# Performance work log

Hardware: AMD Instinct MI355X
Metric: run time of the kernel (lower is better)

The kernel has to match this reference:

```python
import jax, jax.numpy as jnp
import numpy as np

B, T, D, H = 2, 2048, 1024, 16
HD = D // H  # head_dim = 64


def setup_inputs() -> dict:
    key = jax.random.key(0)
    ks = jax.random.split(key, 6)
    x = jax.random.normal(ks[0], (B, T, D), dtype=jnp.float32)
    wq = jax.random.normal(ks[1], (D, D), dtype=jnp.float32) * (D ** -0.5)
    wk = jax.random.normal(ks[2], (D, D), dtype=jnp.float32) * (D ** -0.5)
    wv = jax.random.normal(ks[3], (D, D), dtype=jnp.float32) * (D ** -0.5)
    wo = jax.random.normal(ks[4], (D, D), dtype=jnp.float32) * (D ** -0.5)
    # RoPE tables: standard inverse-frequency angles, shape [T, head_dim]
    inv_freq = 1.0 / (10000.0 ** (jnp.arange(0, HD, 2, dtype=jnp.float32) / HD))
    ang = jnp.arange(T, dtype=jnp.float32)[:, None] * inv_freq[None, :]  # [T, HD/2]
    ang = jnp.concatenate([ang, ang], axis=-1)  # [T, HD]
    cos, sin = jnp.cos(ang), jnp.sin(ang)
    # causal mask [1,1,T,T]: True where attention is allowed
    mask = jnp.tril(jnp.ones((T, T), dtype=bool))[None, None]
    return {"x": x, "wq": wq, "wk": wk, "wv": wv, "wo": wo,
            "cos": cos, "sin": sin, "mask": mask}


def rotate_half(u):
    u1, u2 = jnp.split(u, 2, axis=-1)
    return jnp.concatenate([-u2, u1], axis=-1)


def reference(x, wq, wk, wv, wo, cos, sin, mask):
    b, t, c = x.shape
    # projections (nn.Linear: y = x @ W^T), reshape to [B, H, T, HD]
    def proj(w):
        return (x @ w.T).reshape(b, t, H, HD).transpose(0, 2, 1, 3)
    q, k, v = proj(wq), proj(wk), proj(wv)
    # inline RoPE: cos/sin broadcast [1,1,T,HD]
    co = cos[:t][None, None]
    si = sin[:t][None, None]
    q = q * co + rotate_half(q) * si
    k = k * co + rotate_half(k) * si
    # scaled dot-product attention with causal mask
    att = jnp.einsum("bhqd,bhkd->bhqk", q, k) * (HD ** -0.5)
    att = jnp.where(mask[:, :, :t, :t], att, -jnp.inf)
    att = jax.nn.softmax(att, axis=-1)
    out = jnp.einsum("bhqk,bhkd->bhqd", att, v)
    out = out.transpose(0, 2, 1, 3).reshape(b, t, c)
    return out @ wo.T
```

## Files before the change

### kernel.cpp

```cpp
#include <hip/hip_runtime.h>
#include <hip/hip_bf16.h>
#include <type_traits>

#define B_  2
#define T_  2048
#define D_  1024
#define H_  16
#define HD_ 64

typedef __attribute__((ext_vector_type(8))) short bf16x8;
typedef __attribute__((ext_vector_type(4))) float f32x4;

__device__ __forceinline__ unsigned short f2b(float x) {
  union { __hip_bfloat16 h; unsigned short u; } c;
  c.h = __float2bfloat16(x);
  return c.u;
}
__device__ __forceinline__ float b2f(unsigned short u) {
  union { unsigned short u; __hip_bfloat16 h; } c;
  c.u = u;
  return __bfloat162float(c.h);
}

__device__ __forceinline__ void ld_g2l_16(const unsigned short* g, unsigned short* l) {
  auto gp = (const __attribute__((address_space(1))) unsigned int*)g;
  auto lp = (__attribute__((address_space(3))) unsigned int*)l;
  __builtin_amdgcn_global_load_lds(gp, lp, 16, 0, 0);
}

__global__ void __launch_bounds__(256)
cast_all(const float* __restrict__ x, const float* __restrict__ wq,
         const float* __restrict__ wk, const float* __restrict__ wv,
         const float* __restrict__ wo, unsigned short* __restrict__ xb,
         unsigned short* __restrict__ wp) {
  int blk = blockIdx.x;
  const float* src;
  unsigned short* dst;
  size_t off;
  if (blk < 2048) {
    src = x; dst = xb; off = (size_t)blk * 2048;
  } else {
    int t = (blk - 2048) >> 9;
    int r = (blk - 2048) & 511;
    src = (t == 0) ? wq : (t == 1) ? wk : (t == 2) ? wv : wo;
    dst = wp + (size_t)t * 1048576;
    off = (size_t)r * 2048;
  }
  size_t i = off + threadIdx.x * 8;
  float4 a = *(const float4*)(src + i);
  float4 b = *(const float4*)(src + i + 4);
  unsigned short h[8] = {f2b(a.x), f2b(a.y), f2b(a.z), f2b(a.w),
                         f2b(b.x), f2b(b.y), f2b(b.z), f2b(b.w)};
  *(uint4*)(dst + i) = *(uint4*)h;
}

template <typename OutT, int MROWS>
__device__ __forceinline__ void gemm_core(const unsigned short* __restrict__ A,
                                          const unsigned short* __restrict__ Bw,
                                          OutT* __restrict__ C, int K, int Ldc,
                                          int rope_mode, const float* __restrict__ cosT,
                                          const float* __restrict__ sinT, int tok0) {
  constexpr int MT = MROWS / 32;
  __shared__ unsigned short a_s[2][MROWS * 32];
  __shared__ unsigned short b_s[2][128 * 32];
  const int tid = threadIdx.x;
  const int lane = tid & 63;
  const int w = tid >> 6;
  const int m16 = lane & 15;
  const int quad = lane >> 4;
  const int wm = w >> 1, wn = w & 1;
  const int rl = lane >> 2;
  const int cl = (lane & 3) * 8;

  f32x4 acc[MT][4];
#pragma unroll
  for (int i = 0; i < MT; i++)
#pragma unroll
    for (int j = 0; j < 4; j++) acc[i][j] = (f32x4){0.f, 0.f, 0.f, 0.f};

  auto stage = [&](int it, int bs) {
    int k0 = it * 32;
#pragma unroll
    for (int t = 0; t < MROWS / 64; t++) {
      int seg = w * 16 + t * 64;
      ld_g2l_16(A + (size_t)(seg + rl) * K + k0 + cl, &a_s[bs][seg * 32]);
    }
#pragma unroll
    for (int j2 = 0; j2 < 2; j2++) {
      int seg = w * 32 + j2 * 16;
      ld_g2l_16(Bw + (size_t)(seg + rl) * K + k0 + cl, &b_s[bs][seg * 32]);
    }
  };

  const int nit = K / 32;
  stage(0, 0);
  __syncthreads();
  for (int it = 0; it < nit; it++) {
    int cur = it & 1;
    if (it + 1 < nit) stage(it + 1, cur ^ 1);
    bf16x8 af[MT], bfr[4];
#pragma unroll
    for (int mt = 0; mt < MT; mt++)
      af[mt] = *(const bf16x8*)&a_s[cur][(wm * (MT * 16) + mt * 16 + m16) * 32 + quad * 8];
#pragma unroll
    for (int nt = 0; nt < 4; nt++)
      bfr[nt] = *(const bf16x8*)&b_s[cur][(wn * 64 + nt * 16 + m16) * 32 + quad * 8];
#pragma unroll
    for (int mt = 0; mt < MT; mt++)
#pragma unroll
      for (int nt = 0; nt < 4; nt++)
        acc[mt][nt] = __builtin_amdgcn_mfma_f32_16x16x32_bf16(af[mt], bfr[nt], acc[mt][nt], 0, 0, 0);
    __syncthreads();
  }

  if (rope_mode) {
    float scale = (rope_mode == 2) ? 0.18033688011112042f : 1.f;
#pragma unroll
    for (int mt = 0; mt < MT; mt++)
#pragma unroll
      for (int reg = 0; reg < 4; reg++) {
        int t = (tok0 + wm * (MT * 16) + mt * 16 + quad * 4 + reg) & (T_ - 1);
#pragma unroll
        for (int nt = 0; nt < 2; nt++) {
          int d = nt * 16 + m16;
          float co = cosT[t * HD_ + d] * scale;
          float si = sinT[t * HD_ + d] * scale;
          float lo = acc[mt][nt][reg], hi = acc[mt][nt + 2][reg];
          acc[mt][nt][reg]     = lo * co - hi * si;
          acc[mt][nt + 2][reg] = hi * co + lo * si;
        }
      }
  }
#pragma unroll
  for (int mt = 0; mt < MT; mt++)
#pragma unroll
    for (int nt = 0; nt < 4; nt++)
#pragma unroll
      for (int reg = 0; reg < 4; reg++) {
        OutT* p = C + (size_t)(wm * (MT * 16) + mt * 16 + quad * 4 + reg) * Ldc + wn * 64 + nt * 16 + m16;
        if constexpr (std::is_same_v<OutT, float>) *p = acc[mt][nt][reg];
        else *p = f2b(acc[mt][nt][reg]);
      }
}

__global__ void __launch_bounds__(256)
gemm_qkv(const unsigned short* __restrict__ xb, const unsigned short* __restrict__ wp,
         unsigned short* __restrict__ qkv, const float* __restrict__ cosT,
         const float* __restrict__ sinT) {
  const int nb = blockIdx.x;
  const int bm = blockIdx.y * 128;
  const int mi = nb >> 3;
  const int bn = (nb & 7) * 128;
  const int rope_mode = (mi == 0) ? 2 : (mi == 1) ? 1 : 0;
  gemm_core<unsigned short, 128>(xb + (size_t)bm * D_,
                                 wp + (size_t)(mi * 1024 + bn) * D_,
                                 qkv + (size_t)mi * (4096ull * D_) + (size_t)bm * D_ + bn,
                                 D_, D_, rope_mode, cosT, sinT, bm);
}

__global__ void __launch_bounds__(256)
gemm_out(const unsigned short* __restrict__ Ab, const unsigned short* __restrict__ wob,
         float* __restrict__ C) {
  const int bn = blockIdx.x * 128;
  const int bm = blockIdx.y * 64;
  gemm_core<float, 64>(Ab + (size_t)bm * D_, wob + (size_t)bn * D_,
                       C + (size_t)bm * D_ + bn, D_, D_, 0, nullptr, nullptr, 0);
}

__global__ void __launch_bounds__(256)
vtrans(const unsigned short* __restrict__ V, unsigned short* __restrict__ VT) {
  __shared__ unsigned short tile[64][72];
  const int tid = threadIdx.x;
  const int tb = blockIdx.x, h = blockIdx.y, b = blockIdx.z;
  const unsigned short* Vb = V + ((size_t)b * T_ + tb * 64) * D_ + h * HD_;
  int r = tid >> 2;
  int c = (tid & 3) * 16;
  bf16x8 v0 = *(const bf16x8*)(Vb + (size_t)r * D_ + c);
  bf16x8 v1 = *(const bf16x8*)(Vb + (size_t)r * D_ + c + 8);
#pragma unroll
  for (int e = 0; e < 8; e++) tile[c + e][r] = ((unsigned short*)&v0)[e];
#pragma unroll
  for (int e = 0; e < 8; e++) tile[c + 8 + e][r] = ((unsigned short*)&v1)[e];
  __syncthreads();
  unsigned short* VTb = VT + ((size_t)b * H_ + h) * HD_ * T_ + tb * 64;
  *(bf16x8*)(VTb + (size_t)r * T_ + c)     = *(const bf16x8*)&tile[r][c];
  *(bf16x8*)(VTb + (size_t)r * T_ + c + 8) = *(const bf16x8*)&tile[r][c + 8];
}

__global__ void __launch_bounds__(256, 3)
attn_kernel(const unsigned short* __restrict__ Q, const unsigned short* __restrict__ K,
            const unsigned short* __restrict__ VT, unsigned short* __restrict__ O) {
  __shared__ __align__(16) unsigned short qp_s[64][72];
  __shared__ __align__(16) unsigned short k_s[2][64 * 64];
  __shared__ __align__(16) unsigned short vt_s[2][64 * 64];

  const int tid = threadIdx.x;
  const int lane = tid & 63;
  const int w = tid >> 6;
  const int m16 = lane & 15;
  const int quad = lane >> 4;
  const int swz = m16 & 7;
  const int pc0 = quad ^ swz;
  const int pc1 = pc0 ^ 4;

  const int x = blockIdx.x;
  const int qt = 31 - (x >> 5);
  const int bh = x & 31;
  const int b = bh >> 4, h = bh & 15;
  const int q0 = qt * 64;

  const unsigned short* Qb = Q + ((size_t)b * T_ + q0) * D_ + h * HD_;
  const unsigned short* Kb = K + (size_t)b * T_ * D_ + h * HD_;
  const unsigned short* VTb = VT + ((size_t)b * H_ + h) * HD_ * T_;

#pragma unroll
  for (int i = 0; i < 2; i++) {
    int idx = tid + i * 256;
    int r = idx >> 3, c = idx & 7;
    *(bf16x8*)&qp_s[r][c * 8] = *(const bf16x8*)(Qb + (size_t)r * D_ + c * 8);
  }

  auto stage_kv = [&](int kt, int bs) {
    int rs = lane >> 3;
    int cs = ((lane & 7) ^ rs) * 8;
    int gr = w * 16 + rs;
    ld_g2l_16(Kb + (size_t)(kt * 64 + gr) * D_ + cs,      &k_s[bs][(w * 16) * 64]);
    ld_g2l_16(Kb + (size_t)(kt * 64 + gr + 8) * D_ + cs,  &k_s[bs][(w * 16 + 8) * 64]);
    ld_g2l_16(VTb + (size_t)gr * T_ + kt * 64 + cs,       &vt_s[bs][(w * 16) * 64]);
    ld_g2l_16(VTb + (size_t)(gr + 8) * T_ + kt * 64 + cs, &vt_s[bs][(w * 16 + 8) * 64]);
  };

  f32x4 o_acc[4];
#pragma unroll
  for (int dt = 0; dt < 4; dt++) o_acc[dt] = (f32x4){0.f, 0.f, 0.f, 0.f};
  float m_i = -1e30f, l_i = 0.f;
  const int rg = q0 + w * 16 + m16;

  stage_kv(0, 0);
  __syncthreads();
  bf16x8 q_frag[2];
  q_frag[0] = *(const bf16x8*)&qp_s[w * 16 + m16][quad * 8];
  q_frag[1] = *(const bf16x8*)&qp_s[w * 16 + m16][32 + quad * 8];

  for (int t = 0; t <= qt; t++) {
    int cur = t & 1;
    if (t < qt) stage_kv(t + 1, cur ^ 1);

    const unsigned short* kc = &k_s[cur][0];
    const unsigned short* vc = &vt_s[cur][0];
    f32x4 sf[4];
    __builtin_amdgcn_s_setprio(1);
#pragma unroll
    for (int jt = 0; jt < 4; jt++) {
      bf16x8 a0 = *(const bf16x8*)&kc[(jt * 16 + m16) * 64 + pc0 * 8];
      bf16x8 a1 = *(const bf16x8*)&kc[(jt * 16 + m16) * 64 + pc1 * 8];
      f32x4 acc = (f32x4){0.f, 0.f, 0.f, 0.f};
      acc = __builtin_amdgcn_mfma_f32_16x16x32_bf16(a0, q_frag[0], acc, 0, 0, 0);
      acc = __builtin_amdgcn_mfma_f32_16x16x32_bf16(a1, q_frag[1], acc, 0, 0, 0);
      sf[jt] = acc;
    }
    __builtin_amdgcn_s_setprio(0);
    if (t == qt) {
#pragma unroll
      for (int jt = 0; jt < 4; jt++)
#pragma unroll
        for (int reg = 0; reg < 4; reg++) {
          int jg = t * 64 + jt * 16 + quad * 4 + reg;
          if (jg > rg) sf[jt][reg] = -1e30f;
        }
    }
    float mx = sf[0][0];
#pragma unroll
    for (int jt = 0; jt < 4; jt++)
#pragma unroll
      for (int reg = 0; reg < 4; reg++) mx = fmaxf(mx, sf[jt][reg]);
    mx = fmaxf(mx, __shfl_xor(mx, 16, 64));
    mx = fmaxf(mx, __shfl_xor(mx, 32, 64));
    if (!__all(mx <= m_i + 8.f)) {
      float mn = fmaxf(m_i, mx);
      float alpha = exp2f(m_i - mn);
      l_i *= alpha;
#pragma unroll
      for (int dt = 0; dt < 4; dt++)
#pragma unroll
        for (int reg = 0; reg < 4; reg++) o_acc[dt][reg] *= alpha;
      m_i = mn;
    }
    float lt = 0.f;
    float p[4][4];
#pragma unroll
    for (int jt = 0; jt < 4; jt++)
#pragma unroll
      for (int reg = 0; reg < 4; reg++) {
        p[jt][reg] = exp2f(sf[jt][reg] - m_i);
        lt += p[jt][reg];
      }
#pragma unroll
    for (int jt = 0; jt < 4; jt++) {
      unsigned short pk[4] = {f2b(p[jt][0]), f2b(p[jt][1]), f2b(p[jt][2]), f2b(p[jt][3])};
      *(uint2*)&qp_s[w * 16 + m16][jt * 16 + quad * 4] = *(uint2*)pk;
    }
    bf16x8 bp0 = *(const bf16x8*)&qp_s[w * 16 + m16][quad * 8];
    bf16x8 bp1 = *(const bf16x8*)&qp_s[w * 16 + m16][32 + quad * 8];
    __builtin_amdgcn_s_setprio(1);
#pragma unroll
    for (int dt = 0; dt < 4; dt++) {
      int rowd = dt * 16 + m16;
      bf16x8 a0 = *(const bf16x8*)&vc[rowd * 64 + pc0 * 8];
      bf16x8 a1 = *(const bf16x8*)&vc[rowd * 64 + pc1 * 8];
      o_acc[dt] = __builtin_amdgcn_mfma_f32_16x16x32_bf16(a0, bp0, o_acc[dt], 0, 0, 0);
      o_acc[dt] = __builtin_amdgcn_mfma_f32_16x16x32_bf16(a1, bp1, o_acc[dt], 0, 0, 0);
    }
    __builtin_amdgcn_s_setprio(0);
    lt += __shfl_xor(lt, 16, 64);
    lt += __shfl_xor(lt, 32, 64);
    l_i += lt;
    __syncthreads();
  }

  float inv = 1.f / l_i;
#pragma unroll
  for (int dt = 0; dt < 4; dt++) {
    unsigned short ok[4];
#pragma unroll
    for (int reg = 0; reg < 4; reg++) ok[reg] = f2b(o_acc[dt][reg] * inv);
    *(uint2*)&qp_s[w * 16 + m16][dt * 16 + quad * 4] = *(uint2*)ok;
  }
  __syncthreads();
  unsigned short* Ob = O + ((size_t)b * T_ + q0) * D_ + h * HD_;
#pragma unroll
  for (int i = 0; i < 2; i++) {
    int idx = tid + i * 256;
    int r = idx >> 3, c = idx & 7;
    *(bf16x8*)(Ob + (size_t)r * D_ + c * 8) = *(const bf16x8*)&qp_s[r][c * 8];
  }
}

extern "C" void kernel_launch(void* const* d_in, const int* in_sizes, int n_in,
                              void* d_out, int out_size, void* d_ws, size_t ws_size,
                              hipStream_t stream) {
  const float* x    = (const float*)d_in[0];
  const float* wq   = (const float*)d_in[1];
  const float* wk   = (const float*)d_in[2];
  const float* wv   = (const float*)d_in[3];
  const float* wo   = (const float*)d_in[4];
  const float* cosT = (const float*)d_in[5];
  const float* sinT = (const float*)d_in[6];
  float* out = (float*)d_out;

  const size_t NTOK = (size_t)B_ * T_;
  const size_t SZ   = NTOK * D_;
  unsigned short* xb   = (unsigned short*)d_ws;
  unsigned short* Wp   = xb + SZ;
  unsigned short* QKVh = Wp + 4 * 1048576;
  unsigned short* Ab   = QKVh + 3 * SZ;
  unsigned short* VTb  = xb;

  cast_all<<<4096, 256, 0, stream>>>(x, wq, wk, wv, wo, xb, Wp);
  gemm_qkv<<<dim3(24, 32), 256, 0, stream>>>(xb, Wp, QKVh, cosT, sinT);
  vtrans<<<dim3(32, 16, 2), 256, 0, stream>>>(QKVh + 2 * SZ, VTb);
  attn_kernel<<<1024, 256, 0, stream>>>(QKVh, QKVh + SZ, VTb, Ab);
  gemm_out<<<dim3(8, 64), 256, 0, stream>>>(Ab, Wp + 3 * 1048576, out);
}
```

Measured before the change: 203.2 us.

## Enlarge attention query tile to 128 rows with two sub-tiles per wave

Each attention block now handles 128 query rows instead of 64, and each wave owns 32 rows split into two 16-row sub-tiles. This lets every K/V tile staged in shared memory serve twice as many queries and halves the block count. Block-to-tile mapping is changed to pair long and short causal tiles across the two halves of the grid, and waves whose rows sit entirely before the current key tile skip compute. The cost is more registers per wave, which may lower occupancy, plus uneven per-wave work near the diagonal.

```diff
diff --git a/kernel.cpp b/kernel.cpp
--- a/kernel.cpp
+++ b/kernel.cpp
@@ -190,7 +190,7 @@
 __global__ void __launch_bounds__(256, 3)
 attn_kernel(const unsigned short* __restrict__ Q, const unsigned short* __restrict__ K,
             const unsigned short* __restrict__ VT, unsigned short* __restrict__ O) {
-  __shared__ __align__(16) unsigned short qp_s[64][72];
+  __shared__ __align__(16) unsigned short qp_s[128][72];
   __shared__ __align__(16) unsigned short k_s[2][64 * 64];
   __shared__ __align__(16) unsigned short vt_s[2][64 * 64];
 
@@ -204,20 +204,21 @@
   const int pc1 = pc0 ^ 4;
 
   const int x = blockIdx.x;
-  const int qt = 31 - (x >> 5);
-  const int bh = x & 31;
+  const int c = x & 255, half = x >> 8;
+  const int bh = c & 31, jj = c >> 5;
+  const int qt = half ? jj : 15 - jj;
   const int b = bh >> 4, h = bh & 15;
-  const int q0 = qt * 64;
+  const int q0 = qt * 128;
 
   const unsigned short* Qb = Q + ((size_t)b * T_ + q0) * D_ + h * HD_;
   const unsigned short* Kb = K + (size_t)b * T_ * D_ + h * HD_;
   const unsigned short* VTb = VT + ((size_t)b * H_ + h) * HD_ * T_;
 
 #pragma unroll
-  for (int i = 0; i < 2; i++) {
+  for (int i = 0; i < 4; i++) {
     int idx = tid + i * 256;
-    int r = idx >> 3, c = idx & 7;
-    *(bf16x8*)&qp_s[r][c * 8] = *(const bf16x8*)(Qb + (size_t)r * D_ + c * 8);
+    int r = idx >> 3, cc = idx & 7;
+    *(bf16x8*)&qp_s[r][cc * 8] = *(const bf16x8*)(Qb + (size_t)r * D_ + cc * 8);
   }
 
   auto stage_kv = [&](int kt, int bs) {
@@ -230,109 +231,148 @@
     ld_g2l_16(VTb + (size_t)(gr + 8) * T_ + kt * 64 + cs, &vt_s[bs][(w * 16 + 8) * 64]);
   };
 
-  f32x4 o_acc[4];
-#pragma unroll
-  for (int dt = 0; dt < 4; dt++) o_acc[dt] = (f32x4){0.f, 0.f, 0.f, 0.f};
-  float m_i = -1e30f, l_i = 0.f;
-  const int rg = q0 + w * 16 + m16;
+  f32x4 o_acc[2][4];
+#pragma unroll
+  for (int s = 0; s < 2; s++)
+#pragma unroll
+    for (int dt = 0; dt < 4; dt++) o_acc[s][dt] = (f32x4){0.f, 0.f, 0.f, 0.f};
+  float m_i[2] = {-1e30f, -1e30f}, l_i[2] = {0.f, 0.f};
+  const int rg0 = q0 + w * 32 + m16;
+  const int ktmax = 2 * qt + 1;
 
   stage_kv(0, 0);
   __syncthreads();
-  bf16x8 q_frag[2];
-  q_frag[0] = *(const bf16x8*)&qp_s[w * 16 + m16][quad * 8];
-  q_frag[1] = *(const bf16x8*)&qp_s[w * 16 + m16][32 + quad * 8];
-
-  for (int t = 0; t <= qt; t++) {
+  bf16x8 q_frag[2][2];
+#pragma unroll
+  for (int s = 0; s < 2; s++) {
+    q_frag[s][0] = *(const bf16x8*)&qp_s[w * 32 + s * 16 + m16][quad * 8];
+    q_frag[s][1] = *(const bf16x8*)&qp_s[w * 32 + s * 16 + m16][32 + quad * 8];
+  }
+
+  for (int t = 0; t <= ktmax; t++) {
     int cur = t & 1;
-    if (t < qt) stage_kv(t + 1, cur ^ 1);
-
-    const unsigned short* kc = &k_s[cur][0];
-    const unsigned short* vc = &vt_s[cur][0];
-    f32x4 sf[4];
-    __builtin_amdgcn_s_setprio(1);
-#pragma unroll
-    for (int jt = 0; jt < 4; jt++) {
-      bf16x8 a0 = *(const bf16x8*)&kc[(jt * 16 + m16) * 64 + pc0 * 8];
-      bf16x8 a1 = *(const bf16x8*)&kc[(jt * 16 + m16) * 64 + pc1 * 8];
-      f32x4 acc = (f32x4){0.f, 0.f, 0.f, 0.f};
-      acc = __builtin_amdgcn_mfma_f32_16x16x32_bf16(a0, q_frag[0], acc, 0, 0, 0);
-      acc = __builtin_amdgcn_mfma_f32_16x16x32_bf16(a1, q_frag[1], acc, 0, 0, 0);
-      sf[jt] = acc;
+    if (t < ktmax) stage_kv(t + 1, cur ^ 1);
+
+    if (t * 64 <= q0 + w * 32 + 31) {
+      const unsigned short* kc = &k_s[cur][0];
+      const unsigned short* vc = &vt_s[cur][0];
+      f32x4 sf[2][4];
+      __builtin_amdgcn_s_setprio(1);
+#pragma unroll
+      for (int jt = 0; jt < 4; jt++) {
+        bf16x8 a0 = *(const bf16x8*)&kc[(jt * 16 + m16) * 64 + pc0 * 8];
+        bf16x8 a1 = *(const bf16x8*)&kc[(jt * 16 + m16) * 64 + pc1 * 8];
+#pragma unroll
+        for (int s = 0; s < 2; s++) {
+          f32x4 acc = (f32x4){0.f, 0.f, 0.f, 0.f};
+          acc = __builtin_amdgcn_mfma_f32_16x16x32_bf16(a0, q_frag[s][0], acc, 0, 0, 0);
+          acc = __builtin_amdgcn_mfma_f32_16x16x32_bf16(a1, q_frag[s][1], acc, 0, 0, 0);
+          sf[s][jt] = acc;
+        }
+      }
+      __builtin_amdgcn_s_setprio(0);
+      if (t * 64 + 63 > q0 + w * 32) {
+#pragma unroll
+        for (int s = 0; s < 2; s++) {
+          int rg = rg0 + s * 16;
+#pragma unroll
+          for (int jt = 0; jt < 4; jt++)
+#pragma unroll
+            for (int reg = 0; reg < 4; reg++) {
+              int jg = t * 64 + jt * 16 + quad * 4 + reg;
+              if (jg > rg) sf[s][jt][reg] = -1e30f;
+            }
+        }
+      }
+      float mx[2];
+#pragma unroll
+      for (int s = 0; s < 2; s++) {
+        float m = sf[s][0][0];
+#pragma unroll
+        for (int jt = 0; jt < 4; jt++)
+#pragma unroll
+          for (int reg = 0; reg < 4; reg++) m = fmaxf(m, sf[s][jt][reg]);
+        m = fmaxf(m, __shfl_xor(m, 16, 64));
+        m = fmaxf(m, __shfl_xor(m, 32, 64));
+        mx[s] = m;
+      }
+      if (!__all(fmaxf(mx[0] - m_i[0], mx[1] - m_i[1]) <= 8.f)) {
+#pragma unroll
+        for (int s = 0; s < 2; s++) {
+          float mn = fmaxf(m_i[s], mx[s]);
+          float alpha = exp2f(m_i[s] - mn);
+          l_i[s] *= alpha;
+#pragma unroll
+          for (int dt = 0; dt < 4; dt++)
+#pragma unroll
+            for (int reg = 0; reg < 4; reg++) o_acc[s][dt][reg] *= alpha;
+          m_i[s] = mn;
+        }
+      }
+      float lt[2] = {0.f, 0.f};
+#pragma unroll
+      for (int s = 0; s < 2; s++) {
+        float p[4][4];
+#pragma unroll
+        for (int jt = 0; jt < 4; jt++)
+#pragma unroll
+          for (int reg = 0; reg < 4; reg++) {
+            p[jt][reg] = exp2f(sf[s][jt][reg] - m_i[s]);
+            lt[s] += p[jt][reg];
+          }
+#pragma unroll
+        for (int jt = 0; jt < 4; jt++) {
+          unsigned short pk[4] = {f2b(p[jt][0]), f2b(p[jt][1]), f2b(p[jt][2]), f2b(p[jt][3])};
+          *(uint2*)&qp_s[w * 32 + s * 16 + m16][jt * 16 + quad * 4] = *(uint2*)pk;
+        }
+      }
+      bf16x8 bp[2][2];
+#pragma unroll
+      for (int s = 0; s < 2; s++) {
+        bp[s][0] = *(const bf16x8*)&qp_s[w * 32 + s * 16 + m16][quad * 8];
+        bp[s][1] = *(const bf16x8*)&qp_s[w * 32 + s * 16 + m16][32 + quad * 8];
+      }
+      __builtin_amdgcn_s_setprio(1);
+#pragma unroll
+      for (int dt = 0; dt < 4; dt++) {
+        int rowd = dt * 16 + m16;
+        bf16x8 a0 = *(const bf16x8*)&vc[rowd * 64 + pc0 * 8];
+        bf16x8 a1 = *(const bf16x8*)&vc[rowd * 64 + pc1 * 8];
+#pragma unroll
+        for (int s = 0; s < 2; s++) {
+          o_acc[s][dt] = __builtin_amdgcn_mfma_f32_16x16x32_bf16(a0, bp[s][0], o_acc[s][dt], 0, 0, 0);
+          o_acc[s][dt] = __builtin_amdgcn_mfma_f32_16x16x32_bf16(a1, bp[s][1], o_acc[s][dt], 0, 0, 0);
+        }
+      }
+      __builtin_amdgcn_s_setprio(0);
+#pragma unroll
+      for (int s = 0; s < 2; s++) {
+        lt[s] += __shfl_xor(lt[s], 16, 64);
+        lt[s] += __shfl_xor(lt[s], 32, 64);
+        l_i[s] += lt[s];
+      }
     }
-    __builtin_amdgcn_s_setprio(0);
-    if (t == qt) {
-#pragma unroll
-      for (int jt = 0; jt < 4; jt++)
-#pragma unroll
-        for (int reg = 0; reg < 4; reg++) {
-          int jg = t * 64 + jt * 16 + quad * 4 + reg;
-          if (jg > rg) sf[jt][reg] = -1e30f;
-        }
+    __syncthreads();
+  }
+
+#pragma unroll
+  for (int s = 0; s < 2; s++) {
+    float inv = 1.f / l_i[s];
+#pragma unroll
+    for (int dt = 0; dt < 4; dt++) {
+      unsigned short ok[4];
+#pragma unroll
+      for (int reg = 0; reg < 4; reg++) ok[reg] = f2b(o_acc[s][dt][reg] * inv);
+      *(uint2*)&qp_s[w * 32 + s * 16 + m16][dt * 16 + quad * 4] = *(uint2*)ok;
     }
-    float mx = sf[0][0];
-#pragma unroll
-    for (int jt = 0; jt < 4; jt++)
-#pragma unroll
-      for (int reg = 0; reg < 4; reg++) mx = fmaxf(mx, sf[jt][reg]);
-    mx = fmaxf(mx, __shfl_xor(mx, 16, 64));
-    mx = fmaxf(mx, __shfl_xor(mx, 32, 64));
-    if (!__all(mx <= m_i + 8.f)) {
-      float mn = fmaxf(m_i, mx);
-      float alpha = exp2f(m_i - mn);
-      l_i *= alpha;
-#pragma unroll
-      for (int dt = 0; dt < 4; dt++)
-#pragma unroll
-        for (int reg = 0; reg < 4; reg++) o_acc[dt][reg] *= alpha;
-      m_i = mn;
-    }
-    float lt = 0.f;
-    float p[4][4];
-#pragma unroll
-    for (int jt = 0; jt < 4; jt++)
-#pragma unroll
-      for (int reg = 0; reg < 4; reg++) {
-        p[jt][reg] = exp2f(sf[jt][reg] - m_i);
-        lt += p[jt][reg];
-      }
-#pragma unroll
-    for (int jt = 0; jt < 4; jt++) {
-      unsigned short pk[4] = {f2b(p[jt][0]), f2b(p[jt][1]), f2b(p[jt][2]), f2b(p[jt][3])};
-      *(uint2*)&qp_s[w * 16 + m16][jt * 16 + quad * 4] = *(uint2*)pk;
-    }
-    bf16x8 bp0 = *(const bf16x8*)&qp_s[w * 16 + m16][quad * 8];
-    bf16x8 bp1 = *(const bf16x8*)&qp_s[w * 16 + m16][32 + quad * 8];
-    __builtin_amdgcn_s_setprio(1);
-#pragma unroll
-    for (int dt = 0; dt < 4; dt++) {
-      int rowd = dt * 16 + m16;
-      bf16x8 a0 = *(const bf16x8*)&vc[rowd * 64 + pc0 * 8];
-      bf16x8 a1 = *(const bf16x8*)&vc[rowd * 64 + pc1 * 8];
-      o_acc[dt] = __builtin_amdgcn_mfma_f32_16x16x32_bf16(a0, bp0, o_acc[dt], 0, 0, 0);
-      o_acc[dt] = __builtin_amdgcn_mfma_f32_16x16x32_bf16(a1, bp1, o_acc[dt], 0, 0, 0);
-    }
-    __builtin_amdgcn_s_setprio(0);
-    lt += __shfl_xor(lt, 16, 64);
-    lt += __shfl_xor(lt, 32, 64);
-    l_i += lt;
-    __syncthreads();
-  }
-
-  float inv = 1.f / l_i;
-#pragma unroll
-  for (int dt = 0; dt < 4; dt++) {
-    unsigned short ok[4];
-#pragma unroll
-    for (int reg = 0; reg < 4; reg++) ok[reg] = f2b(o_acc[dt][reg] * inv);
-    *(uint2*)&qp_s[w * 16 + m16][dt * 16 + quad * 4] = *(uint2*)ok;
   }
   __syncthreads();
   unsigned short* Ob = O + ((size_t)b * T_ + q0) * D_ + h * HD_;
 #pragma unroll
-  for (int i = 0; i < 2; i++) {
+  for (int i = 0; i < 4; i++) {
     int idx = tid + i * 256;
-    int r = idx >> 3, c = idx & 7;
-    *(bf16x8*)(Ob + (size_t)r * D_ + c * 8) = *(const bf16x8*)&qp_s[r][c * 8];
+    int r = idx >> 3, cc = idx & 7;
+    *(bf16x8*)(Ob + (size_t)r * D_ + cc * 8) = *(const bf16x8*)&qp_s[r][cc * 8];
   }
 }
 
@@ -359,6 +399,6 @@
   cast_all<<<4096, 256, 0, stream>>>(x, wq, wk, wv, wo, xb, Wp);
   gemm_qkv<<<dim3(24, 32), 256, 0, stream>>>(xb, Wp, QKVh, cosT, sinT);
   vtrans<<<dim3(32, 16, 2), 256, 0, stream>>>(QKVh + 2 * SZ, VTb);
-  attn_kernel<<<1024, 256, 0, stream>>>(QKVh, QKVh + SZ, VTb, Ab);
+  attn_kernel<<<512, 256, 0, stream>>>(QKVh, QKVh + SZ, VTb, Ab);
   gemm_out<<<dim3(8, 64), 256, 0, stream>>>(Ab, Wp + 3 * 1048576, out);
 }
```

After: 222.8 us. +9.7%, slower.
